# Performance work log

Hardware: AMD Instinct MI355X
Metric: run time of the kernel (lower is better)

## Reference

```python
import jax, jax.numpy as jnp
import numpy as np

N_BINS = 15

def setup_inputs() -> dict:
    key = jax.random.key(0)
    k1, k2 = jax.random.split(key)
    N, C = 1048576, 128
    logits = jax.random.normal(k1, (N, C), dtype=jnp.float32)
    labels = jax.random.randint(k2, (N,), 0, C, dtype=jnp.int64)
    return {"logits": logits, "labels": labels}

def reference(logits, labels):
    # softmax + argmax: confidences = max prob, predictions = argmax
    probs = jax.nn.softmax(logits, axis=1)
    conf = jnp.max(probs, axis=1)                      # [N]
    pred = jnp.argmax(probs, axis=1)                   # [N]
    acc = (pred == labels).astype(conf.dtype)          # [N]
    # bin i covers (i/n_bins, (i+1)/n_bins]; conf > 1/C > 0 so ceil-1 lands in-range
    bins = jnp.clip(jnp.ceil(conf * N_BINS).astype(jnp.int32) - 1, 0, N_BINS - 1)
    ones = jnp.ones_like(conf)
    counts = jax.ops.segment_sum(ones, bins, num_segments=N_BINS)
    conf_sum = jax.ops.segment_sum(conf, bins, num_segments=N_BINS)
    acc_sum = jax.ops.segment_sum(acc, bins, num_segments=N_BINS)
    n = jnp.asarray(conf.shape[0], conf.dtype)
    safe = jnp.maximum(counts, 1.0)
    per_bin = jnp.abs(conf_sum / safe - acc_sum / safe) * (counts / n)
    ece = jnp.sum(jnp.where(counts > 0, per_bin, 0.0))
    return ece.reshape(1)
```

## Files before the change

### kernel.cpp

```cpp
#include <hip/hip_runtime.h>

#define N_BINS 15

__global__ __launch_bounds__(256) void ece_main(const float* __restrict__ logits,
                                                const int* __restrict__ labels,
                                                float* __restrict__ ws,
                                                int N) {
    __shared__ float s_counts[N_BINS];
    __shared__ float s_conf[N_BINS];
    __shared__ float s_acc[N_BINS];
    const int tid = threadIdx.x;
    if (tid < N_BINS) { s_counts[tid] = 0.f; s_conf[tid] = 0.f; s_acc[tid] = 0.f; }
    __syncthreads();

    const int lane        = tid & 63;
    const int half        = lane >> 5;
    const int sub         = lane & 31;
    const int waveInBlock = tid >> 6;
    const int rowsPerBlk  = (blockDim.x >> 6) * 2;

    const int rowBase   = blockIdx.x * rowsPerBlk + waveInBlock * 2 + half;
    const int rowStride = gridDim.x * rowsPerBlk;

    for (int row = rowBase; row < N; row += rowStride) {
        const float4* p = (const float4*)(logits + (size_t)row * 128) + sub;
        const float4 v = *p;

        float m = v.x; int mi = sub * 4;
        if (v.y > m) { m = v.y; mi = sub * 4 + 1; }
        if (v.z > m) { m = v.z; mi = sub * 4 + 2; }
        if (v.w > m) { m = v.w; mi = sub * 4 + 3; }

        #pragma unroll
        for (int off = 16; off > 0; off >>= 1) {
            float om = __shfl_xor(m, off);
            int   oi = __shfl_xor(mi, off);
            if (om > m || (om == m && oi < mi)) { m = om; mi = oi; }
        }

        float s = __expf(v.x - m) + __expf(v.y - m) + __expf(v.z - m) + __expf(v.w - m);
        #pragma unroll
        for (int off = 16; off > 0; off >>= 1)
            s += __shfl_xor(s, off);

        if (sub == 0) {
            const float conf = 1.0f / s;
            int bin = (int)ceilf(conf * (float)N_BINS) - 1;
            bin = min(max(bin, 0), N_BINS - 1);
            const float acc = (mi == labels[row]) ? 1.0f : 0.0f;
            atomicAdd(&s_counts[bin], 1.0f);
            atomicAdd(&s_conf[bin],  conf);
            atomicAdd(&s_acc[bin],   acc);
        }
    }
    __syncthreads();
    if (tid < N_BINS) {
        atomicAdd(&ws[tid],              s_counts[tid]);
        atomicAdd(&ws[N_BINS + tid],     s_conf[tid]);
        atomicAdd(&ws[2 * N_BINS + tid], s_acc[tid]);
    }
}

__global__ void ece_final(const float* __restrict__ ws, float* __restrict__ out, float invN) {
    if (threadIdx.x == 0 && blockIdx.x == 0) {
        float ece = 0.f;
        #pragma unroll
        for (int i = 0; i < N_BINS; ++i) {
            const float c = ws[i];
            if (c > 0.f)
                ece += fabsf(ws[N_BINS + i] - ws[2 * N_BINS + i]) * invN;
        }
        out[0] = ece;
    }
}

extern "C" void kernel_launch(void* const* d_in, const int* in_sizes, int n_in,
                              void* d_out, int out_size, void* d_ws, size_t ws_size,
                              hipStream_t stream) {
    const float* logits = (const float*)d_in[0];
    const int*   labels = (const int*)d_in[1];
    float*       out    = (float*)d_out;
    float*       ws     = (float*)d_ws;

    const int N = in_sizes[1];

    hipMemsetAsync(ws, 0, 3 * N_BINS * sizeof(float), stream);

    const int block = 256;
    const int rowsPerBlk = (block >> 6) * 2;
    int grid = 8192;
    if ((size_t)grid * rowsPerBlk > (size_t)N)
        grid = (N + rowsPerBlk - 1) / rowsPerBlk;

    ece_main<<<grid, block, 0, stream>>>(logits, labels, ws, N);
    ece_final<<<1, 64, 0, stream>>>(ws, out, 1.0f / (float)N);
}
```

Baseline: 839.5 us.

## Replace global atomics with per-block partials and load two rows per half-wave

The main kernel now writes per-block bin partials to a workspace array instead of doing global atomicAdds. A 1024-thread final kernel reduces those partials in parallel, which also removes the memset. The grid drops from 8192 to 2048 blocks, and each half-wave issues loads for two rows before processing them, to raise memory-level parallelism. The kernel is bound by memory bandwidth over 512 MB of logits, so any gain depends on better load overlap, and the smaller grid may reduce occupancy-driven latency hiding.

```diff
diff --git a/kernel.cpp b/kernel.cpp
--- a/kernel.cpp
+++ b/kernel.cpp
@@ -1,74 +1,87 @@
 #include <hip/hip_runtime.h>
 
 #define N_BINS 15
+#define GRID_MAIN 2048
+#define BLOCK 256
 
-__global__ __launch_bounds__(256) void ece_main(const float* __restrict__ logits,
-                                                const int* __restrict__ labels,
-                                                float* __restrict__ ws,
-                                                int N) {
-    __shared__ float s_counts[N_BINS];
-    __shared__ float s_conf[N_BINS];
-    __shared__ float s_acc[N_BINS];
+__global__ __launch_bounds__(BLOCK) void ece_main(const float* __restrict__ logits,
+                                                  const int* __restrict__ labels,
+                                                  float* __restrict__ partial,
+                                                  int N, int nBlocks) {
+    __shared__ float s_acc[3 * N_BINS];
     const int tid = threadIdx.x;
-    if (tid < N_BINS) { s_counts[tid] = 0.f; s_conf[tid] = 0.f; s_acc[tid] = 0.f; }
+    if (tid < 3 * N_BINS) s_acc[tid] = 0.f;
     __syncthreads();
 
-    const int lane        = tid & 63;
-    const int half        = lane >> 5;
-    const int sub         = lane & 31;
-    const int waveInBlock = tid >> 6;
-    const int rowsPerBlk  = (blockDim.x >> 6) * 2;
+    const int hw  = tid >> 5;
+    const int sub = tid & 31;
 
-    const int rowBase   = blockIdx.x * rowsPerBlk + waveInBlock * 2 + half;
-    const int rowStride = gridDim.x * rowsPerBlk;
-
-    for (int row = rowBase; row < N; row += rowStride) {
-        const float4* p = (const float4*)(logits + (size_t)row * 128) + sub;
-        const float4 v = *p;
-
+    auto process = [&](const float4 v, int row) {
         float m = v.x; int mi = sub * 4;
         if (v.y > m) { m = v.y; mi = sub * 4 + 1; }
         if (v.z > m) { m = v.z; mi = sub * 4 + 2; }
         if (v.w > m) { m = v.w; mi = sub * 4 + 3; }
-
         #pragma unroll
         for (int off = 16; off > 0; off >>= 1) {
             float om = __shfl_xor(m, off);
             int   oi = __shfl_xor(mi, off);
             if (om > m || (om == m && oi < mi)) { m = om; mi = oi; }
         }
-
         float s = __expf(v.x - m) + __expf(v.y - m) + __expf(v.z - m) + __expf(v.w - m);
         #pragma unroll
         for (int off = 16; off > 0; off >>= 1)
             s += __shfl_xor(s, off);
-
         if (sub == 0) {
             const float conf = 1.0f / s;
             int bin = (int)ceilf(conf * (float)N_BINS) - 1;
             bin = min(max(bin, 0), N_BINS - 1);
             const float acc = (mi == labels[row]) ? 1.0f : 0.0f;
-            atomicAdd(&s_counts[bin], 1.0f);
-            atomicAdd(&s_conf[bin],  conf);
-            atomicAdd(&s_acc[bin],   acc);
+            atomicAdd(&s_acc[bin],              1.0f);
+            atomicAdd(&s_acc[N_BINS + bin],     conf);
+            atomicAdd(&s_acc[2 * N_BINS + bin], acc);
         }
+    };
+
+    const int rowsPerIter = (BLOCK >> 5) * 2;
+    const int rowStride   = nBlocks * rowsPerIter;
+
+    for (int base = blockIdx.x * rowsPerIter + hw * 2; base < N; base += rowStride) {
+        const int r0 = base, r1 = base + 1;
+        const float4 v0 = ((const float4*)(logits + (size_t)r0 * 128))[sub];
+        float4 v1;
+        const bool has1 = (r1 < N);
+        if (has1) v1 = ((const float4*)(logits + (size_t)r1 * 128))[sub];
+        process(v0, r0);
+        if (has1) process(v1, r1);
+    }
+
+    __syncthreads();
+    if (tid < 3 * N_BINS)
+        partial[(size_t)tid * nBlocks + blockIdx.x] = s_acc[tid];
+}
+
+__global__ __launch_bounds__(1024) void ece_final(const float* __restrict__ partial,
+                                                  float* __restrict__ out,
+                                                  int nBlocks, float invN) {
+    __shared__ float red[3 * N_BINS];
+    const int tid = threadIdx.x;
+    const int w = tid >> 6, lane = tid & 63;
+    for (int s = w; s < 3 * N_BINS; s += 16) {
+        float sum = 0.f;
+        for (int i = lane; i < nBlocks; i += 64)
+            sum += partial[(size_t)s * nBlocks + i];
+        #pragma unroll
+        for (int off = 32; off > 0; off >>= 1)
+            sum += __shfl_xor(sum, off);
+        if (lane == 0) red[s] = sum;
     }
     __syncthreads();
-    if (tid < N_BINS) {
-        atomicAdd(&ws[tid],              s_counts[tid]);
-        atomicAdd(&ws[N_BINS + tid],     s_conf[tid]);
-        atomicAdd(&ws[2 * N_BINS + tid], s_acc[tid]);
-    }
-}
-
-__global__ void ece_final(const float* __restrict__ ws, float* __restrict__ out, float invN) {
-    if (threadIdx.x == 0 && blockIdx.x == 0) {
+    if (tid == 0) {
         float ece = 0.f;
         #pragma unroll
-        for (int i = 0; i < N_BINS; ++i) {
-            const float c = ws[i];
-            if (c > 0.f)
-                ece += fabsf(ws[N_BINS + i] - ws[2 * N_BINS + i]) * invN;
+        for (int b = 0; b < N_BINS; ++b) {
+            if (red[b] > 0.f)
+                ece += fabsf(red[N_BINS + b] - red[2 * N_BINS + b]) * invN;
         }
         out[0] = ece;
     }
@@ -80,18 +93,15 @@
     const float* logits = (const float*)d_in[0];
     const int*   labels = (const int*)d_in[1];
     float*       out    = (float*)d_out;
-    float*       ws     = (float*)d_ws;
+    float*       partial = (float*)d_ws;
 
     const int N = in_sizes[1];
 
-    hipMemsetAsync(ws, 0, 3 * N_BINS * sizeof(float), stream);
+    int grid = GRID_MAIN;
+    const int rowsPerIter = (BLOCK >> 5) * 2;
+    if ((size_t)grid * rowsPerIter > (size_t)N)
+        grid = (N + rowsPerIter - 1) / rowsPerIter;
 
-    const int block = 256;
-    const int rowsPerBlk = (block >> 6) * 2;
-    int grid = 8192;
-    if ((size_t)grid * rowsPerBlk > (size_t)N)
-        grid = (N + rowsPerBlk - 1) / rowsPerBlk;
-
-    ece_main<<<grid, block, 0, stream>>>(logits, labels, ws, N);
-    ece_final<<<1, 64, 0, stream>>>(ws, out, 1.0f / (float)N);
+    ece_main<<<grid, BLOCK, 0, stream>>>(logits, labels, partial, N, grid);
+    ece_final<<<1, 1024, 0, stream>>>(partial, out, grid, 1.0f / (float)N);
 }
```

New measurement: 719.9 us. 14.2% less time.
